# Optimization experiments

Hardware: AMD Instinct MI355X
Metric: run time of the kernel (lower is better)

The kernel has to match this reference:

```python
import jax, jax.numpy as jnp
import numpy as np

S, B, E, H, L = 256, 32, 300, 2400, 3


def setup_inputs() -> dict:
    key = jax.random.key(0)
    ks = jax.random.split(key, 8)
    sent = jax.random.normal(ks[0], (S, B, E), dtype=jnp.float32)
    sent_len = jax.random.randint(ks[1], (B,), 1, S + 1, dtype=jnp.int32)
    # QRNN per-layer linear: in_dim -> 3*H (Z, F, O gates), nn.Linear layout [3H, in]
    def lin(k, fan_in):
        s = 1.0 / np.sqrt(fan_in)
        kw, kb = jax.random.split(k)
        W = jax.random.uniform(kw, (3 * H, fan_in), jnp.float32, -s, s)
        b = jax.random.uniform(kb, (3 * H,), jnp.float32, -s, s)
        return W, b
    W1, b1 = lin(ks[2], E)
    W2, b2 = lin(ks[3], H)
    W3, b3 = lin(ks[4], H)
    return {"sent": sent, "sent_len": sent_len,
            "W1": W1, "b1": b1, "W2": W2, "b2": b2, "W3": W3, "b3": b3}


def _qrnn_layer(x, W, b):
    # x: [S, B, D] -> gates [S, B, 3H]
    Y = jnp.einsum('sbd,hd->sbh', x, W) + b
    Z, F, O = jnp.split(Y, 3, axis=-1)
    Z = jnp.tanh(Z)
    F = jax.nn.sigmoid(F)
    O = jax.nn.sigmoid(O)
    c0 = jnp.zeros(Z.shape[1:], Z.dtype)  # [B, H]
    def step(c, zf):
        z, f = zf
        c = f * c + (1.0 - f) * z  # fo-pool elementwise recurrence
        return c, c
    c_last, C = jax.lax.scan(step, c0, (Z, F))
    return O * C, c_last  # hidden seq [S,B,H], final cell [B,H]


def reference(sent, sent_len, W1, b1, W2, b2, W3, b3):
    x = sent
    finals = []
    for (W, b) in ((W1, b1), (W2, b2), (W3, b3)):
        x, c_last = _qrnn_layer(x, W, b)
        finals.append(c_last)
    hidden = jnp.stack(finals, axis=0)  # [L, B, H] == qrnn(...)[1]
    # mean pool as written in the module: sum over dim 0, divide by sent_len
    out = jnp.sum(hidden, axis=0) / sent_len.astype(jnp.float32)[:, None]
    return out  # [B, H]
```

## Files before the change

kernel.cpp:

```cpp
#include <hip/hip_runtime.h>
#include <math.h>
#include <stdint.h>
#include <stddef.h>

#define AS1 __attribute__((address_space(1)))
#define AS3 __attribute__((address_space(3)))

typedef __attribute__((ext_vector_type(8))) __bf16 bf16x8;
typedef __attribute__((ext_vector_type(4))) float f32x4;

#define SQ   256
#define BQ   32
#define EQ   300
#define HQ   2400
#define MQ   (SQ * BQ)
#define N3H  7200
#define N2H  4800
#define KP1  320
#define KP2  2432

__device__ __forceinline__ uint16_t f2bf(float x) {
    uint32_t u = __float_as_uint(x);
    u += 0x7FFFu + ((u >> 16) & 1u);
    return (uint16_t)(u >> 16);
}
__device__ __forceinline__ float bf2f(uint16_t b) {
    return __uint_as_float(((uint32_t)b) << 16);
}
__device__ __forceinline__ float sigm(float x) { return 1.f / (1.f + __expf(-x)); }
__device__ __forceinline__ float tanh_f(float x) { return 2.f / (1.f + __expf(-2.f * x)) - 1.f; }

__global__ void conv_split(const float* __restrict__ src, uint16_t* __restrict__ hi,
                           uint16_t* __restrict__ lo, int rows, int K, int Kp) {
    int idx = blockIdx.x * 256 + threadIdx.x;
    int kp2 = Kp >> 1;
    if (idx >= rows * kp2) return;
    int r = idx / kp2;
    int k = (idx - r * kp2) << 1;
    float2 v = make_float2(0.f, 0.f);
    if (k < K) v = *(const float2*)(src + (size_t)r * K + k);
    uint16_t h0 = f2bf(v.x), h1 = f2bf(v.y);
    uint32_t hw = (uint32_t)h0 | ((uint32_t)h1 << 16);
    uint32_t lw = (uint32_t)f2bf(v.x - bf2f(h0)) | ((uint32_t)f2bf(v.y - bf2f(h1)) << 16);
    size_t o = (size_t)r * Kp + k;
    *(uint32_t*)(hi + o) = hw;
    *(uint32_t*)(lo + o) = lw;
}

__global__ void zero_pad_X(uint16_t* __restrict__ hi, uint16_t* __restrict__ lo) {
    int idx = blockIdx.x * 256 + threadIdx.x;
    if (idx >= MQ * ((KP2 - HQ) >> 1)) return;
    int r = idx >> 4;
    int c = (idx & 15) << 1;
    size_t off = (size_t)r * KP2 + HQ + c;
    *(uint32_t*)(hi + off) = 0u;
    *(uint32_t*)(lo + off) = 0u;
}

template<int KP>
__global__ __launch_bounds__(512, 2) void gemm256(
    const uint16_t* __restrict__ Ahi, const uint16_t* __restrict__ Alo,
    const uint16_t* __restrict__ Whi, const uint16_t* __restrict__ Wlo,
    float* __restrict__ Y, int Ncols, int rowbase)
{
    constexpr int SPS   = KP / 32;
    constexpr int NSLAB = 3 * SPS;
    extern __shared__ char smem[];

    const int tid  = threadIdx.x;
    const int lane = tid & 63;
    const int wave = tid >> 6;
    const int wm   = wave >> 2;
    const int wn   = wave & 3;
    const int lrow0 = blockIdx.y << 8;
    const int col0  = blockIdx.x << 8;
    const int arow0 = rowbase + lrow0;

    const int tq    = tid >> 2;
    const int c_log = (((tid & 3) << 4) ^ ((tq & 3) << 4));
    const int k_el  = c_log >> 1;
    const size_t aofs0 = (size_t)(arow0 + tq) * KP + k_el;
    const size_t aofs1 = (size_t)(arow0 + 128 + tq) * KP + k_el;
    const int wr0 = min(col0 + tq, Ncols - 1);
    const int wr1 = min(col0 + 128 + tq, Ncols - 1);
    const size_t bofs0 = (size_t)wr0 * KP + k_el;
    const size_t bofs1 = (size_t)wr1 * KP + k_el;
    const int ldst = tid << 4;

    const int cphys = (((lane >> 4) << 4) ^ ((lane & 3) << 4));
    const int abase = (((wm << 7) + (lane & 15)) << 6) + cphys;
    const int bbase = (((wn << 6) + (lane & 15)) << 6) + cphys;

    f32x4 acc[8][4];
    {
        f32x4 z = {0.f, 0.f, 0.f, 0.f};
#pragma unroll
        for (int mb = 0; mb < 8; ++mb)
#pragma unroll
            for (int nb = 0; nb < 4; ++nb) acc[mb][nb] = z;
    }

    int sseg = 0, sk0 = 0;
    auto stage = [&](int slot) {
        const uint16_t* Ab = (sseg == 2) ? Alo : Ahi;
        const uint16_t* Bb = (sseg == 1) ? Wlo : Whi;
        char* dst = smem + (slot << 15);
        __builtin_amdgcn_global_load_lds((const AS1 uint32_t*)(Ab + aofs0 + sk0),
                                         (AS3 uint32_t*)(dst + ldst),          16, 0, 0);
        __builtin_amdgcn_global_load_lds((const AS1 uint32_t*)(Ab + aofs1 + sk0),
                                         (AS3 uint32_t*)(dst + 8192  + ldst),  16, 0, 0);
        __builtin_amdgcn_global_load_lds((const AS1 uint32_t*)(Bb + bofs0 + sk0),
                                         (AS3 uint32_t*)(dst + 16384 + ldst),  16, 0, 0);
        __builtin_amdgcn_global_load_lds((const AS1 uint32_t*)(Bb + bofs1 + sk0),
                                         (AS3 uint32_t*)(dst + 24576 + ldst),  16, 0, 0);
        sk0 += 32;
        if (sk0 == KP) { sk0 = 0; ++sseg; }
    };

    auto compute = [&](int slot) {
        const char* sa = smem + (slot << 15);
        const char* sb = sa + 16384;
        bf16x8 af[8], bfr[4];
#pragma unroll
        for (int mb = 0; mb < 8; ++mb) af[mb] = *(const bf16x8*)(sa + abase + (mb << 10));
#pragma unroll
        for (int nb = 0; nb < 4; ++nb) bfr[nb] = *(const bf16x8*)(sb + bbase + (nb << 10));
        __builtin_amdgcn_s_setprio(1);
#pragma unroll
        for (int mb = 0; mb < 8; ++mb)
#pragma unroll
            for (int nb = 0; nb < 4; ++nb)
                acc[mb][nb] = __builtin_amdgcn_mfma_f32_16x16x32_bf16(af[mb], bfr[nb], acc[mb][nb], 0, 0, 0);
        __builtin_amdgcn_s_setprio(0);
    };

    stage(0); stage(1); stage(2);

    for (int j = 0; j < NSLAB - 3; ++j) {
        stage((j + 3) & 3);
        asm volatile("s_waitcnt vmcnt(12)" ::: "memory");
        asm volatile("s_barrier" ::: "memory");
        compute(j & 3);
        asm volatile("s_barrier" ::: "memory");
    }
    asm volatile("s_waitcnt vmcnt(8)" ::: "memory");
    asm volatile("s_barrier" ::: "memory");
    compute((NSLAB - 3) & 3);
    asm volatile("s_waitcnt vmcnt(4)" ::: "memory");
    asm volatile("s_barrier" ::: "memory");
    compute((NSLAB - 2) & 3);
    asm volatile("s_waitcnt vmcnt(0)" ::: "memory");
    asm volatile("s_barrier" ::: "memory");
    compute((NSLAB - 1) & 3);

    const int orow = (lane >> 4) << 2;
    const int ocol = lane & 15;
#pragma unroll
    for (int mb = 0; mb < 8; ++mb) {
        const int r0 = lrow0 + (wm << 7) + (mb << 4) + orow;
#pragma unroll
        for (int nb = 0; nb < 4; ++nb) {
            const int c = col0 + (wn << 6) + (nb << 4) + ocol;
            if (c < Ncols) {
                float* yp = Y + (size_t)r0 * Ncols + c;
#pragma unroll
                for (int r = 0; r < 4; ++r) yp[(size_t)r * Ncols] = acc[mb][nb][r];
            }
        }
    }
}

template<int MODE>
__global__ void scan_k(const float* __restrict__ Y, const float* __restrict__ bias,
                       uint16_t* __restrict__ hhi, uint16_t* __restrict__ hlo,
                       float* __restrict__ cst, float* __restrict__ fin,
                       float* __restrict__ out, const int* __restrict__ slen,
                       int s0, int Sc)
{
    int idx = blockIdx.x * 256 + threadIdx.x;
    if (idx >= BQ * (HQ >> 1)) return;
    int b = idx / (HQ >> 1);
    int h = (idx - b * (HQ >> 1)) << 1;
    const int Ncols = (MODE == 2) ? N2H : N3H;

    const float2 bz = *(const float2*)(bias + h);
    const float2 bg = *(const float2*)(bias + HQ + h);
    const float2 bo = (MODE == 2) ? make_float2(0.f, 0.f) : *(const float2*)(bias + 2 * HQ + h);
    float2 c = (s0 == 0) ? make_float2(0.f, 0.f) : *(const float2*)(cst + b * HQ + h);

    const float* yp = Y + (size_t)b * Ncols + h;
    for (int si = 0; si < Sc; ++si) {
        const float* row = yp + (size_t)si * (BQ * Ncols);
        float2 zr = *(const float2*)(row);
        float2 fr = *(const float2*)(row + HQ);
        float z0 = tanh_f(zr.x + bz.x), z1 = tanh_f(zr.y + bz.y);
        float f0 = sigm(fr.x + bg.x),   f1 = sigm(fr.y + bg.y);
        c.x = f0 * c.x + (1.f - f0) * z0;
        c.y = f1 * c.y + (1.f - f1) * z1;
        if (MODE != 2) {
            float2 orv = *(const float2*)(row + 2 * HQ);
            float o0 = sigm(orv.x + bo.x), o1 = sigm(orv.y + bo.y);
            float h0 = o0 * c.x, h1 = o1 * c.y;
            uint16_t hb0 = f2bf(h0), hb1 = f2bf(h1);
            size_t off = ((size_t)(s0 + si) * BQ + b) * KP2 + h;
            *(uint32_t*)(hhi + off) = (uint32_t)hb0 | ((uint32_t)hb1 << 16);
            *(uint32_t*)(hlo + off) =
                (uint32_t)f2bf(h0 - bf2f(hb0)) | ((uint32_t)f2bf(h1 - bf2f(hb1)) << 16);
        }
    }
    if (s0 + Sc < SQ) {
        *(float2*)(cst + b * HQ + h) = c;
    } else {
        if (MODE == 0) {
            *(float2*)(fin + b * HQ + h) = c;
        } else if (MODE == 1) {
            float2 t = *(const float2*)(fin + b * HQ + h);
            t.x += c.x; t.y += c.y;
            *(float2*)(fin + b * HQ + h) = t;
        } else {
            float inv = 1.f / (float)slen[b];
            float2 t = *(const float2*)(fin + b * HQ + h);
            out[b * HQ + h]     = (t.x + c.x) * inv;
            out[b * HQ + h + 1] = (t.y + c.y) * inv;
        }
    }
}

extern "C" void kernel_launch(void* const* d_in, const int* in_sizes, int n_in,
                              void* d_out, int out_size, void* d_ws, size_t ws_size,
                              hipStream_t stream) {
    const float* sent = (const float*)d_in[0];
    const int*   slen = (const int*)d_in[1];
    const float* Wl[3] = {(const float*)d_in[2], (const float*)d_in[4], (const float*)d_in[6]};
    const float* bl[3] = {(const float*)d_in[3], (const float*)d_in[5], (const float*)d_in[7]};
    float* out = (float*)d_out;

    (void)hipFuncSetAttribute((const void*)gemm256<KP1>,
                              hipFuncAttributeMaxDynamicSharedMemorySize, 131072);
    (void)hipFuncSetAttribute((const void*)gemm256<KP2>,
                              hipFuncAttributeMaxDynamicSharedMemorySize, 131072);

    char* ws = (char*)d_ws;
    uint16_t* A1hi = (uint16_t*)ws;
    uint16_t* A1lo = A1hi + (size_t)MQ * KP1;
    uint16_t* Xhi  = A1lo + (size_t)MQ * KP1;
    uint16_t* Xlo  = Xhi  + (size_t)MQ * KP2;
    uint16_t* Whi  = Xlo  + (size_t)MQ * KP2;
    uint16_t* Wlo  = Whi  + (size_t)N3H * KP2;
    float*    cst  = (float*)(Wlo + (size_t)N3H * KP2);
    float*    fin  = cst + (size_t)BQ * HQ;
    float*    Yc   = fin + (size_t)BQ * HQ;

    const size_t fixed = (size_t)((char*)Yc - ws);
    int Sc = 8;
    const int sc_opts[6] = {256, 128, 64, 32, 16, 8};
    for (int i = 0; i < 6; ++i) {
        size_t need = fixed + (size_t)sc_opts[i] * BQ * N3H * 4 + 256;
        if (need <= ws_size) { Sc = sc_opts[i]; break; }
    }

    conv_split<<<(MQ * (KP1 / 2) + 255) / 256, 256, 0, stream>>>(sent, A1hi, A1lo, MQ, EQ, KP1);
    zero_pad_X<<<(MQ * 16 + 255) / 256, 256, 0, stream>>>(Xhi, Xlo);

    const int sgrid = (BQ * (HQ / 2) + 255) / 256;
    for (int l = 0; l < 3; ++l) {
        const int Ncols = (l == 2) ? N2H : N3H;
        const int Kp    = (l == 0) ? KP1 : KP2;
        const int Ksrc  = (l == 0) ? EQ  : HQ;
        conv_split<<<(Ncols * (Kp / 2) + 255) / 256, 256, 0, stream>>>(Wl[l], Whi, Wlo, Ncols, Ksrc, Kp);
        const uint16_t* Ah = (l == 0) ? A1hi : Xhi;
        const uint16_t* Al = (l == 0) ? A1lo : Xlo;
        dim3 gg((Ncols + 255) / 256, Sc / 8);
        for (int s0 = 0; s0 < SQ; s0 += Sc) {
            if (l == 0)
                gemm256<KP1><<<gg, 512, 131072, stream>>>(Ah, Al, Whi, Wlo, Yc, Ncols, s0 * BQ);
            else
                gemm256<KP2><<<gg, 512, 131072, stream>>>(Ah, Al, Whi, Wlo, Yc, Ncols, s0 * BQ);
            if (l == 0)
                scan_k<0><<<sgrid, 256, 0, stream>>>(Yc, bl[0], Xhi, Xlo, cst, fin, nullptr, nullptr, s0, Sc);
            else if (l == 1)
                scan_k<1><<<sgrid, 256, 0, stream>>>(Yc, bl[1], Xhi, Xlo, cst, fin, nullptr, nullptr, s0, Sc);
            else
                scan_k<2><<<sgrid, 256, 0, stream>>>(Yc, bl[2], nullptr, nullptr, cst, fin, out, slen, s0, Sc);
        }
    }
}
```

Measured before the change: 2.630 ms.

## Fuse split-bf16 passes into one K-loop with XCD-aware block mapping

The GEMM used to stream three separate K passes (hi*hi, hi*lo, lo*hi), reloading the A and B tiles for each. It now loads hi and lo tiles of A and W together per K-slab, double-buffered at 64KB per slot, and issues all three MFMA products from the same LDS data. This cuts global and LDS traffic and the number of barriers. It also remaps the 1D grid so blocks sharing a column tile land on the same XCD for L2 reuse, and changes the LDS swizzle pattern. The pipeline depth drops from 4 stages to 2, so load latency may be less well hidden.

```diff
diff --git a/kernel.cpp b/kernel.cpp
--- a/kernel.cpp
+++ b/kernel.cpp
@@ -61,35 +61,43 @@
 __global__ __launch_bounds__(512, 2) void gemm256(
     const uint16_t* __restrict__ Ahi, const uint16_t* __restrict__ Alo,
     const uint16_t* __restrict__ Whi, const uint16_t* __restrict__ Wlo,
-    float* __restrict__ Y, int Ncols, int rowbase)
+    float* __restrict__ Y, int Ncols, int rowbase, int nrb, int ncb)
 {
-    constexpr int SPS   = KP / 32;
-    constexpr int NSLAB = 3 * SPS;
+    constexpr int NK = KP / 32;
     extern __shared__ char smem[];
+
+    const int d   = blockIdx.x;
+    const int xcd = d & 7;
+    const int rr  = d >> 3;
+    const int row = rr % nrb;
+    const int col = (rr / nrb) * 8 + xcd;
+    if (col >= ncb) return;
+    const int lrow0 = row << 8;
+    const int col0  = col << 8;
+    const int arow0 = rowbase + lrow0;
 
     const int tid  = threadIdx.x;
     const int lane = tid & 63;
     const int wave = tid >> 6;
     const int wm   = wave >> 2;
     const int wn   = wave & 3;
-    const int lrow0 = blockIdx.y << 8;
-    const int col0  = blockIdx.x << 8;
-    const int arow0 = rowbase + lrow0;
-
-    const int tq    = tid >> 2;
-    const int c_log = (((tid & 3) << 4) ^ ((tq & 3) << 4));
-    const int k_el  = c_log >> 1;
-    const size_t aofs0 = (size_t)(arow0 + tq) * KP + k_el;
-    const size_t aofs1 = (size_t)(arow0 + 128 + tq) * KP + k_el;
-    const int wr0 = min(col0 + tq, Ncols - 1);
-    const int wr1 = min(col0 + 128 + tq, Ncols - 1);
-    const size_t bofs0 = (size_t)wr0 * KP + k_el;
-    const size_t bofs1 = (size_t)wr1 * KP + k_el;
+
+    const int tq   = tid >> 2;
+    const int kc   = tid & 3;
+    const int kswz = ((kc ^ ((tq >> 1) & 3)) << 3);
+    const size_t aof0 = (size_t)(arow0 + tq) * KP + kswz;
+    const size_t aof1 = aof0 + (size_t)128 * KP;
+    const int w0 = min(col0 + tq, Ncols - 1);
+    const int w1 = min(col0 + 128 + tq, Ncols - 1);
+    const size_t bof0 = (size_t)w0 * KP + kswz;
+    const size_t bof1 = (size_t)w1 * KP + kswz;
     const int ldst = tid << 4;
 
-    const int cphys = (((lane >> 4) << 4) ^ ((lane & 3) << 4));
-    const int abase = (((wm << 7) + (lane & 15)) << 6) + cphys;
-    const int bbase = (((wn << 6) + (lane & 15)) << 6) + cphys;
+    const int fr    = lane & 15;
+    const int q     = lane >> 4;
+    const int cphys = ((q ^ ((fr >> 1) & 3)) << 4);
+    const int abase = (((wm << 7) + fr) << 6) + cphys;
+    const int bbase = (((wn << 6) + fr) << 6) + cphys;
 
     f32x4 acc[8][4];
     {
@@ -100,58 +108,73 @@
             for (int nb = 0; nb < 4; ++nb) acc[mb][nb] = z;
     }
 
-    int sseg = 0, sk0 = 0;
-    auto stage = [&](int slot) {
-        const uint16_t* Ab = (sseg == 2) ? Alo : Ahi;
-        const uint16_t* Bb = (sseg == 1) ? Wlo : Whi;
-        char* dst = smem + (slot << 15);
-        __builtin_amdgcn_global_load_lds((const AS1 uint32_t*)(Ab + aofs0 + sk0),
-                                         (AS3 uint32_t*)(dst + ldst),          16, 0, 0);
-        __builtin_amdgcn_global_load_lds((const AS1 uint32_t*)(Ab + aofs1 + sk0),
-                                         (AS3 uint32_t*)(dst + 8192  + ldst),  16, 0, 0);
-        __builtin_amdgcn_global_load_lds((const AS1 uint32_t*)(Bb + bofs0 + sk0),
-                                         (AS3 uint32_t*)(dst + 16384 + ldst),  16, 0, 0);
-        __builtin_amdgcn_global_load_lds((const AS1 uint32_t*)(Bb + bofs1 + sk0),
-                                         (AS3 uint32_t*)(dst + 24576 + ldst),  16, 0, 0);
-        sk0 += 32;
-        if (sk0 == KP) { sk0 = 0; ++sseg; }
+    auto stage = [&](int slot, int k0) {
+        char* dst = smem + (slot << 16);
+        __builtin_amdgcn_global_load_lds((const AS1 uint32_t*)(Ahi + aof0 + k0),
+                                         (AS3 uint32_t*)(dst + ldst),                 16, 0, 0);
+        __builtin_amdgcn_global_load_lds((const AS1 uint32_t*)(Ahi + aof1 + k0),
+                                         (AS3 uint32_t*)(dst + 8192  + ldst),         16, 0, 0);
+        __builtin_amdgcn_global_load_lds((const AS1 uint32_t*)(Alo + aof0 + k0),
+                                         (AS3 uint32_t*)(dst + 16384 + ldst),         16, 0, 0);
+        __builtin_amdgcn_global_load_lds((const AS1 uint32_t*)(Alo + aof1 + k0),
+                                         (AS3 uint32_t*)(dst + 16384 + 8192 + ldst),  16, 0, 0);
+        __builtin_amdgcn_global_load_lds((const AS1 uint32_t*)(Whi + bof0 + k0),
+                                         (AS3 uint32_t*)(dst + 32768 + ldst),         16, 0, 0);
+        __builtin_amdgcn_global_load_lds((const AS1 uint32_t*)(Whi + bof1 + k0),
+                                         (AS3 uint32_t*)(dst + 32768 + 8192 + ldst),  16, 0, 0);
+        __builtin_amdgcn_global_load_lds((const AS1 uint32_t*)(Wlo + bof0 + k0),
+                                         (AS3 uint32_t*)(dst + 49152 + ldst),         16, 0, 0);
+        __builtin_amdgcn_global_load_lds((const AS1 uint32_t*)(Wlo + bof1 + k0),
+                                         (AS3 uint32_t*)(dst + 49152 + 8192 + ldst),  16, 0, 0);
     };
 
     auto compute = [&](int slot) {
-        const char* sa = smem + (slot << 15);
-        const char* sb = sa + 16384;
-        bf16x8 af[8], bfr[4];
-#pragma unroll
-        for (int mb = 0; mb < 8; ++mb) af[mb] = *(const bf16x8*)(sa + abase + (mb << 10));
-#pragma unroll
-        for (int nb = 0; nb < 4; ++nb) bfr[nb] = *(const bf16x8*)(sb + bbase + (nb << 10));
+        const char* sa  = smem + (slot << 16);
+        const char* sal = sa + 16384;
+        const char* sbh = sa + 32768;
+        const char* sbl = sa + 49152;
+        bf16x8 a[8], bh[4], bl[4];
+#pragma unroll
+        for (int mb = 0; mb < 8; ++mb) a[mb] = *(const bf16x8*)(sa + abase + (mb << 10));
+#pragma unroll
+        for (int nb = 0; nb < 4; ++nb) bh[nb] = *(const bf16x8*)(sbh + bbase + (nb << 10));
+#pragma unroll
+        for (int nb = 0; nb < 4; ++nb) bl[nb] = *(const bf16x8*)(sbl + bbase + (nb << 10));
         __builtin_amdgcn_s_setprio(1);
 #pragma unroll
         for (int mb = 0; mb < 8; ++mb)
 #pragma unroll
             for (int nb = 0; nb < 4; ++nb)
-                acc[mb][nb] = __builtin_amdgcn_mfma_f32_16x16x32_bf16(af[mb], bfr[nb], acc[mb][nb], 0, 0, 0);
+                acc[mb][nb] = __builtin_amdgcn_mfma_f32_16x16x32_bf16(a[mb], bh[nb], acc[mb][nb], 0, 0, 0);
+#pragma unroll
+        for (int mb = 0; mb < 8; ++mb)
+#pragma unroll
+            for (int nb = 0; nb < 4; ++nb)
+                acc[mb][nb] = __builtin_amdgcn_mfma_f32_16x16x32_bf16(a[mb], bl[nb], acc[mb][nb], 0, 0, 0);
+        __builtin_amdgcn_s_setprio(0);
+#pragma unroll
+        for (int mb = 0; mb < 8; ++mb) a[mb] = *(const bf16x8*)(sal + abase + (mb << 10));
+        __builtin_amdgcn_s_setprio(1);
+#pragma unroll
+        for (int mb = 0; mb < 8; ++mb)
+#pragma unroll
+            for (int nb = 0; nb < 4; ++nb)
+                acc[mb][nb] = __builtin_amdgcn_mfma_f32_16x16x32_bf16(a[mb], bh[nb], acc[mb][nb], 0, 0, 0);
         __builtin_amdgcn_s_setprio(0);
     };
 
-    stage(0); stage(1); stage(2);
-
-    for (int j = 0; j < NSLAB - 3; ++j) {
-        stage((j + 3) & 3);
-        asm volatile("s_waitcnt vmcnt(12)" ::: "memory");
+    stage(0, 0);
+    for (int j = 0; j < NK; ++j) {
+        if (j + 1 < NK) {
+            stage((j + 1) & 1, (j + 1) << 5);
+            asm volatile("s_waitcnt vmcnt(8)" ::: "memory");
+        } else {
+            asm volatile("s_waitcnt vmcnt(0)" ::: "memory");
+        }
         asm volatile("s_barrier" ::: "memory");
-        compute(j & 3);
+        compute(j & 1);
         asm volatile("s_barrier" ::: "memory");
     }
-    asm volatile("s_waitcnt vmcnt(8)" ::: "memory");
-    asm volatile("s_barrier" ::: "memory");
-    compute((NSLAB - 3) & 3);
-    asm volatile("s_waitcnt vmcnt(4)" ::: "memory");
-    asm volatile("s_barrier" ::: "memory");
-    compute((NSLAB - 2) & 3);
-    asm volatile("s_waitcnt vmcnt(0)" ::: "memory");
-    asm volatile("s_barrier" ::: "memory");
-    compute((NSLAB - 1) & 3);
 
     const int orow = (lane >> 4) << 2;
     const int ocol = lane & 15;
@@ -258,6 +281,7 @@
         size_t need = fixed + (size_t)sc_opts[i] * BQ * N3H * 4 + 256;
         if (need <= ws_size) { Sc = sc_opts[i]; break; }
     }
+    const int nrb = Sc / 8;
 
     conv_split<<<(MQ * (KP1 / 2) + 255) / 256, 256, 0, stream>>>(sent, A1hi, A1lo, MQ, EQ, KP1);
     zero_pad_X<<<(MQ * 16 + 255) / 256, 256, 0, stream>>>(Xhi, Xlo);
@@ -270,12 +294,14 @@
         conv_split<<<(Ncols * (Kp / 2) + 255) / 256, 256, 0, stream>>>(Wl[l], Whi, Wlo, Ncols, Ksrc, Kp);
         const uint16_t* Ah = (l == 0) ? A1hi : Xhi;
         const uint16_t* Al = (l == 0) ? A1lo : Xlo;
-        dim3 gg((Ncols + 255) / 256, Sc / 8);
+        const int ncb = (Ncols + 255) / 256;
+        const int cpg = (ncb + 7) / 8;
+        dim3 gg(8 * cpg * nrb);
         for (int s0 = 0; s0 < SQ; s0 += Sc) {
             if (l == 0)
-                gemm256<KP1><<<gg, 512, 131072, stream>>>(Ah, Al, Whi, Wlo, Yc, Ncols, s0 * BQ);
+                gemm256<KP1><<<gg, 512, 131072, stream>>>(Ah, Al, Whi, Wlo, Yc, Ncols, s0 * BQ, nrb, ncb);
             else
-                gemm256<KP2><<<gg, 512, 131072, stream>>>(Ah, Al, Whi, Wlo, Yc, Ncols, s0 * BQ);
+                gemm256<KP2><<<gg, 512, 131072, stream>>>(Ah, Al, Whi, Wlo, Yc, Ncols, s0 * BQ, nrb, ncb);
             if (l == 0)
                 scan_k<0><<<sgrid, 256, 0, stream>>>(Yc, bl[0], Xhi, Xlo, cst, fin, nullptr, nullptr, s0, Sc);
             else if (l == 1)
```

New measurement: 2.199 ms. -16.4%, faster.
